# Kernel tuning notes

Measured on AMD Instinct MI355X. Metric: run time of the kernel, lower is better.

The kernel has to match this reference:

```python
import jax, jax.numpy as jnp
import numpy as np

C = 256
CK = C // 8  # qk projection dim


def setup_inputs() -> dict:
    key = jax.random.key(0)
    ks = jax.random.split(key, 8)
    B, H, W = 4, 64, 64
    x = jax.random.normal(ks[0], (B, C, W, H), dtype=jnp.float32)
    s = 1.0 / np.sqrt(C)
    Wf = jax.random.normal(ks[1], (CK, C), dtype=jnp.float32) * s
    bf = jax.random.normal(ks[2], (CK,), dtype=jnp.float32) * 0.01
    Wg = jax.random.normal(ks[3], (CK, C), dtype=jnp.float32) * s
    bg = jax.random.normal(ks[4], (CK,), dtype=jnp.float32) * 0.01
    Wh = jax.random.normal(ks[5], (C, C), dtype=jnp.float32) * s
    bh = jax.random.normal(ks[6], (C,), dtype=jnp.float32) * 0.01
    gamma = jax.random.normal(ks[7], (1,), dtype=jnp.float32) * 0.1
    return {"x": x, "Wf": Wf, "bf": bf, "Wg": Wg, "bg": bg,
            "Wh": Wh, "bh": bh, "gamma": gamma}


def reference(x, Wf, bf, Wg, bg, Wh, bh, gamma):
    B, Cc, Wd, Hd = x.shape
    N = Wd * Hd
    xf = x.reshape(B, Cc, N)  # B C N
    # 1x1 conv1d == channel matmul
    f = jnp.einsum('oc,bcn->bon', Wf, xf) + bf[None, :, None]  # B CK N
    g = jnp.einsum('oc,bcn->bon', Wg, xf) + bg[None, :, None]  # B CK N
    h = jnp.einsum('oc,bcn->bon', Wh, xf) + bh[None, :, None]  # B C N
    # s[b,i,j] = sum_k f[b,k,i] g[b,k,j]
    s = jnp.einsum('bki,bkj->bij', f, g)  # B N N
    attention = jax.nn.softmax(s, axis=-1)
    # out[b,c,i] = sum_j h[b,c,j] attention[b,i,j]
    out = jnp.einsum('bcj,bij->bci', h, attention)  # B C N
    out = out.reshape(B, Cc, Wd, Hd)
    return gamma[0] * out + x
```

## Files before the change

### kernel.cpp

```cpp
#include <hip/hip_runtime.h>

typedef __bf16 bf16x8 __attribute__((ext_vector_type(8)));
typedef __bf16 bf16x4 __attribute__((ext_vector_type(4)));
typedef float f32x4 __attribute__((ext_vector_type(4)));
typedef float f32x16 __attribute__((ext_vector_type(16)));

__device__ __forceinline__ f32x4 mfma16(bf16x8 a, bf16x8 b, f32x4 c) {
  return __builtin_amdgcn_mfma_f32_16x16x32_bf16(a, b, c, 0, 0, 0);
}
__device__ __forceinline__ f32x16 mfma32(bf16x8 a, bf16x8 b, f32x16 c) {
  return __builtin_amdgcn_mfma_f32_32x32x16_bf16(a, b, c, 0, 0, 0);
}

__device__ __forceinline__ unsigned int cvtpk(float a, float b) {
  union { __bf16 h[2]; unsigned int u; } r;
  r.h[0] = (__bf16)a; r.h[1] = (__bf16)b;
  return r.u;
}
__device__ __forceinline__ void swap32(unsigned int &a, unsigned int &b) {
  asm("v_permlane32_swap_b32 %0, %1" : "+v"(a), "+v"(b));
}

__device__ __forceinline__ void sync_lds() {
  asm volatile("s_waitcnt lgkmcnt(0)" ::: "memory");
  __builtin_amdgcn_s_barrier();
}

__device__ __forceinline__ void pack_tile(const f32x16 s, float &rs,
                                          bf16x8 &A0v, bf16x8 &A1v) {
  float p[16];
#pragma unroll
  for (int r = 0; r < 16; r++) { p[r] = exp2f(s[r]); rs += p[r]; }
  unsigned int a0 = cvtpk(p[0], p[1]), a1 = cvtpk(p[2], p[3]);
  unsigned int a2 = cvtpk(p[4], p[5]), a3 = cvtpk(p[6], p[7]);
  swap32(a0, a2); swap32(a1, a3);
  unsigned int a4 = cvtpk(p[8], p[9]), a5 = cvtpk(p[10], p[11]);
  unsigned int a6 = cvtpk(p[12], p[13]), a7 = cvtpk(p[14], p[15]);
  swap32(a4, a6); swap32(a5, a7);
  union { unsigned int u[4]; bf16x8 v; } A0, A1;
  A0.u[0] = a0; A0.u[1] = a1; A0.u[2] = a2; A0.u[3] = a3;
  A1.u[0] = a4; A1.u[1] = a5; A1.u[2] = a6; A1.u[3] = a7;
  A0v = A0.v; A1v = A1.v;
}

__global__ void wcvt_kernel(const float* __restrict__ Wf, const float* __restrict__ Wg,
                            const float* __restrict__ Wh, __bf16* __restrict__ Wb) {
  int i = blockIdx.x * 256 + threadIdx.x;
  float v;
  if (i < 8192)       v = Wf[i];
  else if (i < 16384) v = Wg[i - 8192];
  else                v = Wh[i - 16384];
  Wb[i] = (__bf16)v;
}

__global__ __launch_bounds__(512) void proj_kernel(
    const float* __restrict__ x, const float* __restrict__ bfv,
    const float* __restrict__ bgv, const float* __restrict__ bhv,
    const __bf16* __restrict__ Wb, __bf16* __restrict__ qkpk,
    __bf16* __restrict__ vpk) {
  __shared__ __align__(16) char smem[2560 + 18432];
  __bf16* xT = (__bf16*)smem;
  __bf16* ho = (__bf16*)(smem + 2560);

  const int t = threadIdx.x;
  const int l = t & 63, wg = t >> 6, q = l >> 4, l15 = l & 15;
  const int nh = wg & 1, oh = wg >> 1;
  const int bi = blockIdx.x;
  const int b = bi >> 7;
  const int nt = bi & 127;
  const int n0 = nt << 5;

  const float* xb = x + (size_t)b * 256 * 4096;

  f32x4 acc[5];
#pragma unroll
  for (int i = 0; i < 5; i++) acc[i] = (f32x4){0.f, 0.f, 0.f, 0.f};

  const int c_rel = t >> 4;
  const int n2 = (t & 15) * 2;

#pragma unroll 1
  for (int kc = 0; kc < 8; kc++) {
    __syncthreads();
    float2 v = *(const float2*)(xb + (size_t)(kc * 32 + c_rel) * 4096 + n0 + n2);
    xT[(n2 + 0) * 40 + c_rel] = (__bf16)v.x;
    xT[(n2 + 1) * 40 + c_rel] = (__bf16)v.y;
    __syncthreads();
    bf16x8 af = *(const bf16x8*)(xT + (nh * 16 + l15) * 40 + q * 8);
    const __bf16* wp = Wb + (size_t)(oh * 80 + l15) * 256 + kc * 32 + q * 8;
#pragma unroll
    for (int ot = 0; ot < 5; ot++) {
      bf16x8 bfr = *(const bf16x8*)(wp + (size_t)ot * 16 * 256);
      acc[ot] = mfma16(af, bfr, acc[ot]);
    }
  }

#pragma unroll
  for (int ot = 0; ot < 5; ot++) {
    int o = oh * 80 + ot * 16 + l15;
    float bias = (o < 32) ? bfv[o] : (o < 64) ? bgv[o - 32] : bhv[o - 64];
    if (oh == 0 && ot < 4) {
      int qk = o >> 5, fr = (o >> 4) & 1, hh = (o >> 3) & 1, e = o & 7;
      size_t base = ((size_t)b * 128 + nt) * 2048 + qk * 1024 + fr * 512 + hh * 256;
      float sc = (o >= 32) ? 1.44269504089f : 1.0f;
#pragma unroll
      for (int r = 0; r < 4; r++) {
        int n_rel = nh * 16 + q * 4 + r;
        qkpk[base + n_rel * 8 + e] = (__bf16)((acc[ot][r] + bias) * sc);
      }
    } else {
#pragma unroll
      for (int r = 0; r < 4; r++) {
        int n_rel = nh * 16 + q * 4 + r;
        ho[(o - 64) * 36 + n_rel] = (__bf16)(acc[ot][r] + bias);
      }
    }
  }
  __syncthreads();
  unsigned short* vpku = (unsigned short*)vpk + (size_t)b * 1048576;
  const unsigned short* hou = (const unsigned short*)ho;
  for (int e = t; e < 4096; e += 512) {
    int c = e >> 4, nn = (e & 15) * 2;
    int n = n0 + nn;
    int jc = n >> 4, hh = (n >> 3) & 1, ee = n & 7;
    unsigned int vv = *(const unsigned int*)(hou + c * 36 + nn);
    *(unsigned int*)(vpku + (((size_t)(jc * 2 + hh) * 256 + c) * 8 + ee)) = vv;
  }
}

__global__ __launch_bounds__(512, 2) void attn_kernel(
    const __bf16* __restrict__ qkpk, const __bf16* __restrict__ vpk,
    __bf16* __restrict__ pO, float* __restrict__ Lp) {
  __shared__ __align__(16) char smem[139264];
  __bf16* Vbuf = (__bf16*)smem;

  const int t = threadIdx.x;
  const int l = t & 63, w = t >> 6;
  const int h = l >> 5, l31 = l & 31;

  const int bi = blockIdx.x;
  const int xcd = bi & 7;
  const int combo = xcd * 2 + ((bi >> 3) & 1);
  const int ig = bi >> 4;
  const int b = combo >> 2, jp = combo & 3;
  const int ti = ig * 8 + w;
  const int n0 = ti << 5;

  const __bf16* qkb = qkpk + (size_t)b * 262144;
  const __bf16* vpb = vpk + (size_t)b * 1048576;
  const int jq0 = jp << 10;

  const __bf16* qp = qkb + (size_t)ti * 2048 + h * 256 + l31 * 8;
  const bf16x8 qf0 = *(const bf16x8*)(qp);
  const bf16x8 qf1 = *(const bf16x8*)(qp + 512);

  f32x16 acc[8] = {};
  float rsum = 0.f;

  const __bf16* kbase = qkb + 1024 + h * 256 + l31 * 8;
  const int vfo = h * 2048 + l31 * 8;

  bf16x8 pac0, pac1;
  {
    const __bf16* src = vpb + (size_t)(jq0 >> 4) * 4096;
    bf16x8 sa = *(const bf16x8*)(src + t * 8);
    bf16x8 sc = *(const bf16x8*)(src + 4096 + t * 8);

    bf16x8 k0 = *(const bf16x8*)(kbase + (size_t)(jq0 >> 5) * 2048);
    bf16x8 k1 = *(const bf16x8*)(kbase + (size_t)(jq0 >> 5) * 2048 + 512);
    f32x16 s = {};
    s = mfma32(k0, qf0, s);
    s = mfma32(k1, qf1, s);
    pack_tile(s, rsum, pac0, pac1);

    *(bf16x8*)(Vbuf + t * 8) = sa;
    *(bf16x8*)(Vbuf + 4096 + t * 8) = sc;
  }
  bf16x8 kf0 = *(const bf16x8*)(kbase + (size_t)((jq0 >> 5) + 1) * 2048);
  bf16x8 kf1 = *(const bf16x8*)(kbase + (size_t)((jq0 >> 5) + 1) * 2048 + 512);
  sync_lds();

#pragma unroll 1
  for (int ch = 0; ch < 32; ++ch) {
    bf16x8 sv0, sv1;
    if (ch < 31) {
      const __bf16* src = vpb + (size_t)((jq0 >> 4) + (ch + 1) * 2) * 4096;
      sv0 = *(const bf16x8*)(src + t * 8);
      sv1 = *(const bf16x8*)(src + 4096 + t * 8);
    }

    f32x16 s_next = {};
    if (ch < 31) {
      s_next = mfma32(kf0, qf0, s_next);
      s_next = mfma32(kf1, qf1, s_next);
    }
    if (ch < 30) {
      const __bf16* kp = kbase + (size_t)((jq0 >> 5) + ch + 2) * 2048;
      kf0 = *(const bf16x8*)(kp);
      kf1 = *(const bf16x8*)(kp + 512);
    }

    const __bf16* rb = Vbuf + (ch & 1) * 8192;

#pragma unroll
    for (int ct = 0; ct < 8; ct++) {
      bf16x8 vv = *(const bf16x8*)(rb + vfo + ct * 256);
      acc[ct] = mfma32(pac0, vv, acc[ct]);
    }

    bf16x8 pan0, pan1;
    if (ch < 31) pack_tile(s_next, rsum, pan0, pan1);

#pragma unroll
    for (int ct = 0; ct < 8; ct++) {
      bf16x8 vv = *(const bf16x8*)(rb + 4096 + vfo + ct * 256);
      acc[ct] = mfma32(pac1, vv, acc[ct]);
    }

    if (ch < 31) {
      pac0 = pan0; pac1 = pan1;
      __bf16* wb = Vbuf + ((ch + 1) & 1) * 8192;
      *(bf16x8*)(wb + t * 8) = sv0;
      *(bf16x8*)(wb + 4096 + t * 8) = sv1;
    }
    sync_lds();
  }

  __bf16* stage = (__bf16*)smem + (size_t)w * 8704;
#pragma unroll
  for (int ct = 0; ct < 8; ct++) {
    int c0 = ct * 32 + l31;
#pragma unroll
    for (int r = 0; r < 16; r++) {
      int i_loc = (r & 3) + 8 * (r >> 2) + 4 * h;
      stage[c0 * 34 + i_loc] = (__bf16)acc[ct][r];
    }
  }
  asm volatile("s_waitcnt lgkmcnt(0)" ::: "memory");

  unsigned short* ob = (unsigned short*)pO + (size_t)(jp * 4 + b) * 1048576 + n0;
  const unsigned short* su = (const unsigned short*)stage;
#pragma unroll 1
  for (int e = l; e < 4096; e += 64) {
    int c = e >> 4, i2 = (e & 15) * 2;
    unsigned int vv = *(const unsigned int*)(su + c * 34 + i2);
    *(unsigned int*)(ob + (size_t)c * 4096 + i2) = vv;
  }

  rsum += __shfl_xor(rsum, 32);
  if (l < 32) Lp[(size_t)(jp * 4 + b) * 4096 + n0 + l] = rsum;
}

__global__ __launch_bounds__(256) void norm_kernel(
    const float* __restrict__ x, const float* __restrict__ gamma_p,
    const __bf16* __restrict__ pO, const float* __restrict__ Lp,
    float* __restrict__ out) {
  const int bc = blockIdx.x;
  const int b = bc >> 8;
  const float gm = gamma_p[0];
  const float* xr = x + (size_t)bc * 4096;
  float* orow = out + (size_t)bc * 4096;
  const __bf16* pbase = pO + (size_t)bc * 4096;
  const float* lbase = Lp + (size_t)b * 4096;

  for (int i0 = threadIdx.x * 4; i0 < 4096; i0 += 1024) {
    float4 xv = *(const float4*)(xr + i0);
    float s0 = 0.f, s1 = 0.f, s2 = 0.f, s3 = 0.f;
    float l0 = 0.f, l1 = 0.f, l2 = 0.f, l3 = 0.f;
#pragma unroll
    for (int jp = 0; jp < 4; jp++) {
      bf16x4 pv = *(const bf16x4*)(pbase + (size_t)jp * 4194304 + i0);
      s0 += (float)pv[0]; s1 += (float)pv[1]; s2 += (float)pv[2]; s3 += (float)pv[3];
      float4 lv = *(const float4*)(lbase + (size_t)jp * 16384 + i0);
      l0 += lv.x; l1 += lv.y; l2 += lv.z; l3 += lv.w;
    }
    float4 ov;
    ov.x = gm * s0 / l0 + xv.x;
    ov.y = gm * s1 / l1 + xv.y;
    ov.z = gm * s2 / l2 + xv.z;
    ov.w = gm * s3 / l3 + xv.w;
    *(float4*)(orow + i0) = ov;
  }
}

extern "C" void kernel_launch(void* const* d_in, const int* in_sizes, int n_in,
                              void* d_out, int out_size, void* d_ws, size_t ws_size,
                              hipStream_t stream) {
  const float* x   = (const float*)d_in[0];
  const float* Wf  = (const float*)d_in[1];
  const float* bfv = (const float*)d_in[2];
  const float* Wg  = (const float*)d_in[3];
  const float* bgv = (const float*)d_in[4];
  const float* Wh  = (const float*)d_in[5];
  const float* bhv = (const float*)d_in[6];
  const float* gm  = (const float*)d_in[7];
  float* out = (float*)d_out;

  char* ws = (char*)d_ws;
  __bf16* Wb   = (__bf16*)ws;
  __bf16* qkpk = (__bf16*)(ws + 262144);
  __bf16* vpk  = (__bf16*)(ws + 2359296);
  __bf16* pO   = (__bf16*)(ws + 10747904);
  float*  Lp   = (float*)(ws + 44302336);

  hipLaunchKernelGGL(wcvt_kernel, dim3(320), dim3(256), 0, stream, Wf, Wg, Wh, Wb);
  hipLaunchKernelGGL(proj_kernel, dim3(512), dim3(512), 0, stream,
                     x, bfv, bgv, bhv, Wb, qkpk, vpk);
  hipLaunchKernelGGL(attn_kernel, dim3(256), dim3(512), 0, stream,
                     qkpk, vpk, pO, Lp);
  hipLaunchKernelGGL(norm_kernel, dim3(1024), dim3(256), 0, stream,
                     x, gm, pO, Lp, out);
}
```

Before: 170.4 us.

## Halve attention block size and shrink shared memory to raise occupancy

```diff
diff --git a/kernel.cpp b/kernel.cpp
--- a/kernel.cpp
+++ b/kernel.cpp
@@ -128,10 +128,10 @@
   }
 }
 
-__global__ __launch_bounds__(512, 2) void attn_kernel(
+__global__ __launch_bounds__(256, 2) void attn_kernel(
     const __bf16* __restrict__ qkpk, const __bf16* __restrict__ vpk,
     __bf16* __restrict__ pO, float* __restrict__ Lp) {
-  __shared__ __align__(16) char smem[139264];
+  __shared__ __align__(16) char smem[34816];
   __bf16* Vbuf = (__bf16*)smem;
 
   const int t = threadIdx.x;
@@ -143,7 +143,7 @@
   const int combo = xcd * 2 + ((bi >> 3) & 1);
   const int ig = bi >> 4;
   const int b = combo >> 2, jp = combo & 3;
-  const int ti = ig * 8 + w;
+  const int ti = ig * 4 + w;
   const int n0 = ti << 5;
 
   const __bf16* qkb = qkpk + (size_t)b * 262144;
@@ -160,91 +160,82 @@
   const __bf16* kbase = qkb + 1024 + h * 256 + l31 * 8;
   const int vfo = h * 2048 + l31 * 8;
 
-  bf16x8 pac0, pac1;
+  bf16x8 kf0 = *(const bf16x8*)(kbase + (size_t)(jq0 >> 5) * 2048);
+  bf16x8 kf1 = *(const bf16x8*)(kbase + (size_t)(jq0 >> 5) * 2048 + 512);
+
   {
     const __bf16* src = vpb + (size_t)(jq0 >> 4) * 4096;
-    bf16x8 sa = *(const bf16x8*)(src + t * 8);
-    bf16x8 sc = *(const bf16x8*)(src + 4096 + t * 8);
-
-    bf16x8 k0 = *(const bf16x8*)(kbase + (size_t)(jq0 >> 5) * 2048);
-    bf16x8 k1 = *(const bf16x8*)(kbase + (size_t)(jq0 >> 5) * 2048 + 512);
-    f32x16 s = {};
-    s = mfma32(k0, qf0, s);
-    s = mfma32(k1, qf1, s);
-    pack_tile(s, rsum, pac0, pac1);
-
-    *(bf16x8*)(Vbuf + t * 8) = sa;
-    *(bf16x8*)(Vbuf + 4096 + t * 8) = sc;
-  }
-  bf16x8 kf0 = *(const bf16x8*)(kbase + (size_t)((jq0 >> 5) + 1) * 2048);
-  bf16x8 kf1 = *(const bf16x8*)(kbase + (size_t)((jq0 >> 5) + 1) * 2048 + 512);
+#pragma unroll
+    for (int s = 0; s < 4; s++)
+      *(bf16x8*)(Vbuf + s * 2048 + t * 8) = *(const bf16x8*)(src + s * 2048 + t * 8);
+  }
   sync_lds();
 
 #pragma unroll 1
   for (int ch = 0; ch < 32; ++ch) {
-    bf16x8 sv0, sv1;
+    bf16x8 sv[4];
     if (ch < 31) {
       const __bf16* src = vpb + (size_t)((jq0 >> 4) + (ch + 1) * 2) * 4096;
-      sv0 = *(const bf16x8*)(src + t * 8);
-      sv1 = *(const bf16x8*)(src + 4096 + t * 8);
-    }
-
-    f32x16 s_next = {};
+#pragma unroll
+      for (int s = 0; s < 4; s++)
+        sv[s] = *(const bf16x8*)(src + s * 2048 + t * 8);
+    }
+
+    f32x16 s = {};
+    s = mfma32(kf0, qf0, s);
+    s = mfma32(kf1, qf1, s);
+
     if (ch < 31) {
-      s_next = mfma32(kf0, qf0, s_next);
-      s_next = mfma32(kf1, qf1, s_next);
-    }
-    if (ch < 30) {
-      const __bf16* kp = kbase + (size_t)((jq0 >> 5) + ch + 2) * 2048;
+      const __bf16* kp = kbase + (size_t)((jq0 >> 5) + ch + 1) * 2048;
       kf0 = *(const bf16x8*)(kp);
       kf1 = *(const bf16x8*)(kp + 512);
     }
 
+    bf16x8 pa0, pa1;
+    pack_tile(s, rsum, pa0, pa1);
+
     const __bf16* rb = Vbuf + (ch & 1) * 8192;
-
 #pragma unroll
     for (int ct = 0; ct < 8; ct++) {
       bf16x8 vv = *(const bf16x8*)(rb + vfo + ct * 256);
-      acc[ct] = mfma32(pac0, vv, acc[ct]);
-    }
-
-    bf16x8 pan0, pan1;
-    if (ch < 31) pack_tile(s_next, rsum, pan0, pan1);
-
+      acc[ct] = mfma32(pa0, vv, acc[ct]);
+    }
 #pragma unroll
     for (int ct = 0; ct < 8; ct++) {
       bf16x8 vv = *(const bf16x8*)(rb + 4096 + vfo + ct * 256);
-      acc[ct] = mfma32(pac1, vv, acc[ct]);
+      acc[ct] = mfma32(pa1, vv, acc[ct]);
     }
 
     if (ch < 31) {
-      pac0 = pan0; pac1 = pan1;
       __bf16* wb = Vbuf + ((ch + 1) & 1) * 8192;
-      *(bf16x8*)(wb + t * 8) = sv0;
-      *(bf16x8*)(wb + 4096 + t * 8) = sv1;
+#pragma unroll
+      for (int s = 0; s < 4; s++)
+        *(bf16x8*)(wb + s * 2048 + t * 8) = sv[s];
     }
     sync_lds();
   }
 
-  __bf16* stage = (__bf16*)smem + (size_t)w * 8704;
-#pragma unroll
-  for (int ct = 0; ct < 8; ct++) {
-    int c0 = ct * 32 + l31;
-#pragma unroll
-    for (int r = 0; r < 16; r++) {
-      int i_loc = (r & 3) + 8 * (r >> 2) + 4 * h;
-      stage[c0 * 34 + i_loc] = (__bf16)acc[ct][r];
-    }
-  }
-  asm volatile("s_waitcnt lgkmcnt(0)" ::: "memory");
-
+  __bf16* stage = (__bf16*)smem + (size_t)w * 4352;
   unsigned short* ob = (unsigned short*)pO + (size_t)(jp * 4 + b) * 1048576 + n0;
   const unsigned short* su = (const unsigned short*)stage;
 #pragma unroll 1
-  for (int e = l; e < 4096; e += 64) {
-    int c = e >> 4, i2 = (e & 15) * 2;
-    unsigned int vv = *(const unsigned int*)(su + c * 34 + i2);
-    *(unsigned int*)(ob + (size_t)c * 4096 + i2) = vv;
+  for (int half = 0; half < 2; half++) {
+#pragma unroll
+    for (int ct2 = 0; ct2 < 4; ct2++) {
+      int c0 = ct2 * 32 + l31;
+#pragma unroll
+      for (int r = 0; r < 16; r++) {
+        int i_loc = (r & 3) + 8 * (r >> 2) + 4 * h;
+        stage[c0 * 34 + i_loc] = (__bf16)acc[half * 4 + ct2][r];
+      }
+    }
+    asm volatile("s_waitcnt lgkmcnt(0)" ::: "memory");
+#pragma unroll 1
+    for (int e = l; e < 2048; e += 64) {
+      int c = e >> 4, i2 = (e & 15) * 2;
+      unsigned int vv = *(const unsigned int*)(su + c * 34 + i2);
+      *(unsigned int*)(ob + (size_t)(half * 128 + c) * 4096 + i2) = vv;
+    }
   }
 
   rsum += __shfl_xor(rsum, 32);
@@ -306,7 +297,7 @@
   hipLaunchKernelGGL(wcvt_kernel, dim3(320), dim3(256), 0, stream, Wf, Wg, Wh, Wb);
   hipLaunchKernelGGL(proj_kernel, dim3(512), dim3(512), 0, stream,
                      x, bfv, bgv, bhv, Wb, qkpk, vpk);
-  hipLaunchKernelGGL(attn_kernel, dim3(256), dim3(512), 0, stream,
+  hipLaunchKernelGGL(attn_kernel, dim3(512), dim3(256), 0, stream,
                      qkpk, vpk, pO, Lp);
   hipLaunchKernelGGL(norm_kernel, dim3(1024), dim3(256), 0, stream,
                      x, gm, pO, Lp, out);
```

Measured after the change: 189.7 us. 1.11x slower.
